# Performance work log

Hardware: AMD Instinct MI355X
Metric: run time of the kernel (lower is better)

The kernel has to match this reference:

```python
import jax, jax.numpy as jnp
import numpy as np

N_NODES = 50000
N_EDGES = 600000
N_GRAPHS = 64
IN_D, HID, EMB = 5, 128, 64
BN_EPS = 1e-5


def setup_inputs() -> dict:
    key = jax.random.key(0)
    ks = jax.random.split(key, 16)
    x = jax.random.normal(ks[0], (N_NODES, IN_D), dtype=jnp.float32)
    src = jax.random.randint(ks[1], (N_EDGES,), 0, N_NODES, dtype=jnp.int32)
    dst = jax.random.randint(ks[2], (N_EDGES,), 0, N_NODES, dtype=jnp.int32)
    batch = jnp.sort(jax.random.randint(ks[3], (N_NODES,), 0, N_GRAPHS, dtype=jnp.int32))
    def lin(k, fi, fo):
        s = 1.0 / np.sqrt(fi)
        kw, kb = jax.random.split(k)
        return (jax.random.uniform(kw, (fi, fo), jnp.float32, -s, s),
                jax.random.uniform(kb, (fo,), jnp.float32, -s, s))
    W1, b1 = lin(ks[4], IN_D, HID)
    W2, b2 = lin(ks[5], HID, HID)
    W3, b3 = lin(ks[6], HID, HID)
    Wp, bp = lin(ks[7], HID, EMB)
    g1 = 1.0 + 0.1 * jax.random.normal(ks[8], (HID,), jnp.float32)
    g2 = 1.0 + 0.1 * jax.random.normal(ks[9], (HID,), jnp.float32)
    g3 = 1.0 + 0.1 * jax.random.normal(ks[10], (HID,), jnp.float32)
    be1 = 0.1 * jax.random.normal(ks[11], (HID,), jnp.float32)
    be2 = 0.1 * jax.random.normal(ks[12], (HID,), jnp.float32)
    be3 = 0.1 * jax.random.normal(ks[13], (HID,), jnp.float32)
    return dict(x=x, src=src, dst=dst, batch=batch,
                W1=W1, b1=b1, W2=W2, b2=b2, W3=W3, b3=b3,
                g1=g1, be1=be1, g2=g2, be2=be2, g3=g3, be3=be3,
                Wp=Wp, bp=bp)


def reference(x, src, dst, batch, W1, b1, W2, b2, W3, b3,
              g1, be1, g2, be2, g3, be3, Wp, bp):
    n = x.shape[0]
    # GCNConv with self-loops and symmetric normalization (PyG default)
    loop = jnp.arange(n, dtype=src.dtype)
    s = jnp.concatenate([src, loop])
    d = jnp.concatenate([dst, loop])
    deg = jax.ops.segment_sum(jnp.ones_like(d, dtype=x.dtype), d, num_segments=n)
    dinv = jnp.where(deg > 0, jax.lax.rsqrt(deg), 0.0)
    norm = (dinv[s] * dinv[d])[:, None]  # (E+N, 1)

    def gcn(h, W, b):
        hw = h @ W                                   # (N, HID)
        msg = hw[s] * norm                           # gather + scale
        agg = jax.ops.segment_sum(msg, d, num_segments=n)
        return agg + b

    def bn_relu(h, g, be):
        # eval-mode BatchNorm1d with running_mean=0, running_var=1
        return jax.nn.relu(h * (g * jax.lax.rsqrt(jnp.asarray(1.0 + BN_EPS, h.dtype))) + be)

    h = bn_relu(gcn(x, W1, b1), g1, be1)
    h = bn_relu(gcn(h, W2, b2), g2, be2)
    h = bn_relu(gcn(h, W3, b3), g3, be3)

    # global mean pool over graphs
    sums = jax.ops.segment_sum(h, batch, num_segments=N_GRAPHS)
    cnt = jax.ops.segment_sum(jnp.ones((n,), h.dtype), batch, num_segments=N_GRAPHS)
    pooled = sums / jnp.maximum(cnt, 1.0)[:, None]
    return pooled @ Wp + bp
```

## Files before the change

kernel.cpp:

```cpp
#include <hip/hip_runtime.h>
#include <hip/hip_fp16.h>

#define N_NODES 50000
#define N_EDGES 600000
#define N_GRAPHS 64
#define IN_D 5
#define HID 128
#define EMB 64

#define CHUNK 512
#define NCHUNK ((N_NODES + CHUNK - 1) / CHUNK)
#define NREP 16
#define NLOC 4

typedef _Float16 half8 __attribute__((ext_vector_type(8)));
typedef float float4v __attribute__((ext_vector_type(4)));


__global__ __launch_bounds__(256) void k_init(
        int* __restrict__ cnt, int* __restrict__ fill, float* __restrict__ psum_rep,
        const float* __restrict__ W2, const float* __restrict__ W3,
        _Float16* __restrict__ Wt2, _Float16* __restrict__ Wt3) {
    int tid = blockIdx.x * blockDim.x + threadIdx.x;
    int nt = gridDim.x * blockDim.x;
    for (int i = tid; i < N_NODES; i += nt) { cnt[i] = 0; fill[i] = 0; }
    for (int i = tid; i < NREP * N_GRAPHS * HID; i += nt) psum_rep[i] = 0.f;
    for (int i = tid; i < 2 * HID * HID; i += nt) {
        int rem = i & (HID * HID - 1);
        int k = rem & 127, f = rem >> 7;
        if (i < HID * HID) Wt2[rem] = (_Float16)W2[k * HID + f];
        else               Wt3[rem] = (_Float16)W3[k * HID + f];
    }
}


__global__ __launch_bounds__(256) void k_count(
        const int* __restrict__ dst, int* __restrict__ cnt) {
    int e = blockIdx.x * blockDim.x + threadIdx.x;
    if (e < N_EDGES) atomicAdd(&cnt[dst[e]], 1);
}


__global__ void k_chunksum(const int* __restrict__ cnt, int* __restrict__ csum,
                           float* __restrict__ dinv) {
    __shared__ int sh[256];
    int b = blockIdx.x, t = threadIdx.x;
    int i0 = b * CHUNK + t, i1 = i0 + 256;
    int v = 0;
    if (i0 < N_NODES) { int c = cnt[i0]; v += c; dinv[i0] = rsqrtf((float)c + 1.0f); }
    if (i1 < N_NODES) { int c = cnt[i1]; v += c; dinv[i1] = rsqrtf((float)c + 1.0f); }
    sh[t] = v; __syncthreads();
    for (int off = 128; off > 0; off >>= 1) {
        if (t < off) sh[t] += sh[t + off];
        __syncthreads();
    }
    if (t == 0) csum[b] = sh[0];
}


__global__ void k_scan(const int* __restrict__ cnt, const int* __restrict__ csum,
                       int* __restrict__ row_start) {
    __shared__ int ws[4];
    int b = blockIdx.x, t = threadIdx.x;
    int lane = t & 63, w = t >> 6;

    int pre = 0;
    for (int j = lane; j < b; j += 64) pre += csum[j];
    #pragma unroll
    for (int off = 32; off > 0; off >>= 1) pre += __shfl_down(pre, off);
    pre = __shfl(pre, 0);

    int base = b * CHUNK;
    int i0 = base + 2 * t, i1 = i0 + 1;
    int c0 = (i0 < N_NODES) ? cnt[i0] : 0;
    int c1 = (i1 < N_NODES) ? cnt[i1] : 0;
    int v = c0 + c1;
    int s = v;
    #pragma unroll
    for (int off = 1; off < 64; off <<= 1) {
        int u = __shfl_up(s, off);
        if (lane >= off) s += u;
    }
    if (lane == 63) ws[w] = s;
    __syncthreads();
    if (t == 0) {
        int r = 0;
        #pragma unroll
        for (int j = 0; j < 4; ++j) { int xx = ws[j]; ws[j] = r; r += xx; }
    }
    __syncthreads();
    int excl = s - v + ws[w] + pre;
    if (i0 < N_NODES) row_start[i0] = excl;
    if (i1 < N_NODES) row_start[i1] = excl + c0;
    if (b == 0 && t == 0) row_start[N_NODES] = N_EDGES;
}


__global__ __launch_bounds__(256) void k_scatter(
        const int* __restrict__ src, const int* __restrict__ dst,
        const float* __restrict__ dinv, const int* __restrict__ row_start,
        int* __restrict__ fill, int2* __restrict__ e_pack) {
    int e = blockIdx.x * blockDim.x + threadIdx.x;
    if (e >= N_EDGES) return;
    int d = dst[e];
    int pos = row_start[d] + atomicAdd(&fill[d], 1);
    int s = src[e];
    e_pack[pos] = make_int2(s, __float_as_int(dinv[s]));
}


__global__ __launch_bounds__(256) void k_agg5g1(
        const float* __restrict__ x, const float* __restrict__ dinv,
        const int* __restrict__ row_start, const int2* __restrict__ e_pack,
        const float* __restrict__ W1, const float* __restrict__ b1,
        const float* __restrict__ g1, const float* __restrict__ be1,
        __half2* __restrict__ H16) {
    int gid = blockIdx.x * blockDim.x + threadIdx.x;
    int i = gid >> 3, k = gid & 7;
    if (i >= N_NODES) return;
    float acc = 0.f;
    if (k < IN_D) {
        int beg = row_start[i], end = row_start[i + 1];
        int e = beg;
        for (; e + 3 < end; e += 4) {
            int2 p0 = e_pack[e];
            int2 p1 = e_pack[e + 1];
            int2 p2 = e_pack[e + 2];
            int2 p3 = e_pack[e + 3];
            float x0 = x[p0.x * IN_D + k];
            float x1 = x[p1.x * IN_D + k];
            float x2 = x[p2.x * IN_D + k];
            float x3 = x[p3.x * IN_D + k];
            acc = fmaf(__int_as_float(p0.y), x0, acc);
            acc = fmaf(__int_as_float(p1.y), x1, acc);
            acc = fmaf(__int_as_float(p2.y), x2, acc);
            acc = fmaf(__int_as_float(p3.y), x3, acc);
        }
        for (; e < end; ++e) {
            int2 p = e_pack[e];
            acc = fmaf(__int_as_float(p.y), x[p.x * IN_D + k], acc);
        }
        float di = dinv[i];
        acc = di * (acc + di * x[i * IN_D + k]);
    }
    int lane = threadIdx.x & 63;
    int base = lane & ~7;
    float a0 = __shfl(acc, base + 0);
    float a1 = __shfl(acc, base + 1);
    float a2 = __shfl(acc, base + 2);
    float a3 = __shfl(acc, base + 3);
    float a4 = __shfl(acc, base + 4);
    const float rs = rsqrtf(1.0f + 1e-5f);
    int f0 = k * 16;
    #pragma unroll
    for (int u = 0; u < 8; ++u) {
        int fa = f0 + u * 2, fb = fa + 1;
        float va = b1[fa], vb = b1[fb];
        va = fmaf(a0, W1[0 * HID + fa], va); vb = fmaf(a0, W1[0 * HID + fb], vb);
        va = fmaf(a1, W1[1 * HID + fa], va); vb = fmaf(a1, W1[1 * HID + fb], vb);
        va = fmaf(a2, W1[2 * HID + fa], va); vb = fmaf(a2, W1[2 * HID + fb], vb);
        va = fmaf(a3, W1[3 * HID + fa], va); vb = fmaf(a3, W1[3 * HID + fb], vb);
        va = fmaf(a4, W1[4 * HID + fa], va); vb = fmaf(a4, W1[4 * HID + fb], vb);
        va = fmaf(va, g1[fa] * rs, be1[fa]);
        vb = fmaf(vb, g1[fb] * rs, be1[fb]);
        va = va > 0.f ? va : 0.f;
        vb = vb > 0.f ? vb : 0.f;
        H16[(size_t)i * 64 + k * 8 + u] = __floats2half2_rn(va, vb);
    }
}


__global__ __launch_bounds__(256) void k_agg128h(
        const __half2* __restrict__ H2, const float* __restrict__ dinv,
        const int* __restrict__ row_start, const int2* __restrict__ e_pack,
        __half2* __restrict__ A16) {
    int n = (blockIdx.x * blockDim.x + threadIdx.x) >> 6;
    int lane = threadIdx.x & 63;
    if (n >= N_NODES) return;
    float2 acc = make_float2(0.f, 0.f);
    int beg = row_start[n], end = row_start[n + 1];
    int e = beg;
    for (; e + 7 < end; e += 8) {
        int2 p[8];
        float2 h[8];
        #pragma unroll
        for (int u = 0; u < 8; ++u) p[u] = e_pack[e + u];
        #pragma unroll
        for (int u = 0; u < 8; ++u)
            h[u] = __half22float2(H2[(size_t)p[u].x * 64 + lane]);
        #pragma unroll
        for (int u = 0; u < 8; ++u) {
            float w = __int_as_float(p[u].y);
            acc.x = fmaf(w, h[u].x, acc.x);
            acc.y = fmaf(w, h[u].y, acc.y);
        }
    }
    for (; e + 3 < end; e += 4) {
        int2 p[4];
        float2 h[4];
        #pragma unroll
        for (int u = 0; u < 4; ++u) p[u] = e_pack[e + u];
        #pragma unroll
        for (int u = 0; u < 4; ++u)
            h[u] = __half22float2(H2[(size_t)p[u].x * 64 + lane]);
        #pragma unroll
        for (int u = 0; u < 4; ++u) {
            float w = __int_as_float(p[u].y);
            acc.x = fmaf(w, h[u].x, acc.x);
            acc.y = fmaf(w, h[u].y, acc.y);
        }
    }
    for (; e < end; ++e) {
        int2 pe = e_pack[e];
        float w = __int_as_float(pe.y);
        float2 f = __half22float2(H2[(size_t)pe.x * 64 + lane]);
        acc.x = fmaf(w, f.x, acc.x);
        acc.y = fmaf(w, f.y, acc.y);
    }
    float di = dinv[n];
    float2 hs = __half22float2(H2[(size_t)n * 64 + lane]);
    acc.x = fmaf(di, hs.x, acc.x);
    acc.y = fmaf(di, hs.y, acc.y);
    A16[(size_t)n * 64 + lane] = __floats2half2_rn(di * acc.x, di * acc.y);
}


__global__ __launch_bounds__(256) void k_gemm2(
        const _Float16* __restrict__ A16, const _Float16* __restrict__ Wt,
        const float* __restrict__ bb, const float* __restrict__ gg,
        const float* __restrict__ bee, _Float16* __restrict__ outH) {
    int t = threadIdx.x;
    int w = t >> 6, lane = t & 63;
    int quad = lane >> 4, r16 = lane & 15;
    int nb = blockIdx.x * 64 + w * 16;
    const float rs = rsqrtf(1.0f + 1e-5f);
    const half8* Arow = (const half8*)(A16 + (size_t)(nb + r16) * 128);
    half8 a[4];
    #pragma unroll
    for (int kb = 0; kb < 4; ++kb) a[kb] = Arow[kb * 4 + quad];
    #pragma unroll
    for (int ft = 0; ft < 8; ++ft) {
        int f = ft * 16 + r16;
        const half8* Brow = (const half8*)(Wt + (size_t)f * 128);
        float4v acc = {0.f, 0.f, 0.f, 0.f};
        #pragma unroll
        for (int kb = 0; kb < 4; ++kb)
            acc = __builtin_amdgcn_mfma_f32_16x16x32_f16(a[kb], Brow[kb * 4 + quad],
                                                         acc, 0, 0, 0);
        float b0 = bb[f], g0 = gg[f] * rs, e0 = bee[f];
        #pragma unroll
        for (int rr = 0; rr < 4; ++rr) {
            int n = nb + quad * 4 + rr;
            if (n < N_NODES) {
                float v = fmaf(acc[rr] + b0, g0, e0);
                v = v > 0.f ? v : 0.f;
                outH[(size_t)n * 128 + f] = (_Float16)v;
            }
        }
    }
}


__global__ __launch_bounds__(256) void k_gemm3pool(
        const _Float16* __restrict__ A16, const _Float16* __restrict__ Wt,
        const float* __restrict__ bb, const float* __restrict__ gg,
        const float* __restrict__ bee, const int* __restrict__ batch,
        float* __restrict__ psum_rep) {
    __shared__ float sh_pool[NLOC][HID];
    int t = threadIdx.x;
    int w = t >> 6, lane = t & 63;
    int quad = lane >> 4, r16 = lane & 15;
    int blk = (int)blockIdx.x;
    int nb = blk * 64 + w * 16;
    const float rs = rsqrtf(1.0f + 1e-5f);

    for (int i = t; i < NLOC * HID; i += 256) ((float*)sh_pool)[i] = 0.f;

    const half8* Arow = (const half8*)(A16 + (size_t)(nb + r16) * 128);
    half8 a[4];
    #pragma unroll
    for (int kb = 0; kb < 4; ++kb) a[kb] = Arow[kb * 4 + quad];

    int nb0 = blk * 64;
    if (nb0 > N_NODES - 1) nb0 = N_NODES - 1;
    int g0 = batch[nb0];
    int gi4[4];
    #pragma unroll
    for (int rr = 0; rr < 4; ++rr) {
        int n = nb + quad * 4 + rr;
        gi4[rr] = (n < N_NODES) ? batch[n] : -1;
    }
    __syncthreads();

    float* rep = psum_rep + (size_t)(blk & (NREP - 1)) * N_GRAPHS * HID;

    #pragma unroll
    for (int ft = 0; ft < 8; ++ft) {
        int f = ft * 16 + r16;
        const half8* Brow = (const half8*)(Wt + (size_t)f * 128);
        float4v acc = {0.f, 0.f, 0.f, 0.f};
        #pragma unroll
        for (int kb = 0; kb < 4; ++kb)
            acc = __builtin_amdgcn_mfma_f32_16x16x32_f16(a[kb], Brow[kb * 4 + quad],
                                                         acc, 0, 0, 0);
        float b0 = bb[f], g0f = gg[f] * rs, e0 = bee[f];
        float partial = 0.f;
        int cur = -1;
        #pragma unroll
        for (int rr = 0; rr < 4; ++rr) {
            int gi = gi4[rr];
            if (gi >= 0) {
                float v = fmaf(acc[rr] + b0, g0f, e0);
                v = v > 0.f ? v : 0.f;
                if (gi != cur) {
                    if (cur >= 0) {
                        int idx = cur - g0;
                        if (idx < NLOC) atomicAdd(&sh_pool[idx][f], partial);
                        else            atomicAdd(&rep[cur * HID + f], partial);
                    }
                    partial = 0.f; cur = gi;
                }
                partial += v;
            }
        }
        if (cur >= 0) {
            int idx = cur - g0;
            if (idx < NLOC) atomicAdd(&sh_pool[idx][f], partial);
            else            atomicAdd(&rep[cur * HID + f], partial);
        }
    }
    __syncthreads();
    for (int i = t; i < NLOC * HID; i += 256) {
        int idx = i >> 7, f = i & 127;
        float v = sh_pool[idx][f];
        int g = g0 + idx;
        if (v != 0.f && g < N_GRAPHS) atomicAdd(&rep[g * HID + f], v);
    }
}


__device__ __forceinline__ int lower_bound_batch(const int* __restrict__ batch, int val) {
    int lo = 0, hi = N_NODES;
    while (lo < hi) {
        int mid = (lo + hi) >> 1;
        if (batch[mid] < val) lo = mid + 1;
        else hi = mid;
    }
    return lo;
}

__global__ void k_final(const float* __restrict__ psum_rep, const int* __restrict__ batch,
                        const float* __restrict__ Wp, const float* __restrict__ bp,
                        float* __restrict__ out) {
    __shared__ float s_p[HID];
    int gi = blockIdx.x, e = threadIdx.x;
    for (int f = e; f < HID; f += EMB) {
        float v = 0.f;
        #pragma unroll
        for (int r = 0; r < NREP; ++r)
            v += psum_rep[(size_t)r * N_GRAPHS * HID + gi * HID + f];
        s_p[f] = v;
    }
    int lane = e & 63;
    int r = 0;
    if (lane < 2) r = lower_bound_batch(batch, gi + lane);
    int c0 = __shfl(r, 0), c1 = __shfl(r, 1);
    float inv = 1.0f / fmaxf((float)(c1 - c0), 1.0f);
    __syncthreads();
    float acc = bp[e];
    #pragma unroll 8
    for (int f = 0; f < HID; ++f)
        acc = fmaf(s_p[f] * inv, Wp[f * EMB + e], acc);
    out[gi * EMB + e] = acc;
}


extern "C" void kernel_launch(void* const* d_in, const int* in_sizes, int n_in,
                              void* d_out, int out_size, void* d_ws, size_t ws_size,
                              hipStream_t stream) {
    const float* x   = (const float*)d_in[0];
    const int*   src = (const int*)d_in[1];
    const int*   dst = (const int*)d_in[2];
    const int* batch = (const int*)d_in[3];
    const float* W1 = (const float*)d_in[4];
    const float* b1 = (const float*)d_in[5];
    const float* W2 = (const float*)d_in[6];
    const float* b2 = (const float*)d_in[7];
    const float* W3 = (const float*)d_in[8];
    const float* b3 = (const float*)d_in[9];
    const float* g1 = (const float*)d_in[10];
    const float* be1 = (const float*)d_in[11];
    const float* g2 = (const float*)d_in[12];
    const float* be2 = (const float*)d_in[13];
    const float* g3 = (const float*)d_in[14];
    const float* be3 = (const float*)d_in[15];
    const float* Wp = (const float*)d_in[16];
    const float* bp = (const float*)d_in[17];
    float* out = (float*)d_out;

    char* ws = (char*)d_ws;
    size_t o = 0;
    auto alloc = [&](size_t bytes) {
        void* pp = ws + o;
        o += bytes;
        o = (o + 255) & ~255ull;
        return pp;
    };
    int*      cnt       = (int*)alloc(N_NODES * 4);
    int*      fill      = (int*)alloc(N_NODES * 4);
    int*      row_start = (int*)alloc((N_NODES + 1) * 4);
    int*      csum      = (int*)alloc(NCHUNK * 4);
    float*    dinv      = (float*)alloc(N_NODES * 4);
    int2*     e_pack    = (int2*)alloc((size_t)N_EDGES * 8);
    _Float16* Wt2       = (_Float16*)alloc(HID * HID * 2);
    _Float16* Wt3       = (_Float16*)alloc(HID * HID * 2);
    __half2*  H16       = (__half2*)alloc((size_t)(N_NODES + 64) * HID * 2);
    __half2*  A16       = (__half2*)alloc((size_t)(N_NODES + 64) * HID * 2);
    float*    psum_rep  = (float*)alloc((size_t)NREP * N_GRAPHS * HID * 4);

    k_init<<<512, 256, 0, stream>>>(cnt, fill, psum_rep, W2, W3, Wt2, Wt3);
    k_count<<<(N_EDGES + 255) / 256, 256, 0, stream>>>(dst, cnt);
    k_chunksum<<<NCHUNK, 256, 0, stream>>>(cnt, csum, dinv);
    k_scan<<<NCHUNK, 256, 0, stream>>>(cnt, csum, row_start);
    k_scatter<<<(N_EDGES + 255) / 256, 256, 0, stream>>>(src, dst, dinv, row_start,
                                                         fill, e_pack);
    k_agg5g1<<<(N_NODES * 8 + 255) / 256, 256, 0, stream>>>(x, dinv, row_start, e_pack,
                                                            W1, b1, g1, be1, H16);
    k_agg128h<<<(N_NODES * 64 + 255) / 256, 256, 0, stream>>>(H16, dinv, row_start,
                                                              e_pack, A16);
    k_gemm2<<<(N_NODES + 63) / 64, 256, 0, stream>>>((const _Float16*)A16, Wt2,
                                                     b2, g2, be2, (_Float16*)H16);
    k_agg128h<<<(N_NODES * 64 + 255) / 256, 256, 0, stream>>>(H16, dinv, row_start,
                                                              e_pack, A16);
    k_gemm3pool<<<(N_NODES + 63) / 64, 256, 0, stream>>>((const _Float16*)A16, Wt3,
                                                         b3, g3, be3, batch, psum_rep);
    k_final<<<N_GRAPHS, EMB, 0, stream>>>(psum_rep, batch, Wp, bp, out);
}
```

Before: 293.9 us.

## Fuse 128-wide aggregation with MFMA GEMM through LDS and merge scan kernels

Each block now aggregates 64 nodes' neighbour features into padded shared memory and feeds them directly to the MFMA GEMM with BN/ReLU (and pooling in the last layer). This removes the A16 intermediate round-trip to global memory and two launches. The chunk-sum and scan kernels are merged into one kernel that recomputes prefixes directly, and init work is folded in alongside a memset. The cost is that each wave processes its 16 rows sequentially in the gather phase, which gives less memory parallelism per wave than the old one-node-per-wave layout, and the prefix loop is quadratic in the number of chunks.

```diff
diff --git a/kernel.cpp b/kernel.cpp
--- a/kernel.cpp
+++ b/kernel.cpp
@@ -12,26 +12,11 @@
 #define NCHUNK ((N_NODES + CHUNK - 1) / CHUNK)
 #define NREP 16
 #define NLOC 4
+#define RSTRIDE_H 136
 
 typedef _Float16 half8 __attribute__((ext_vector_type(8)));
+typedef _Float16 half2v __attribute__((ext_vector_type(2)));
 typedef float float4v __attribute__((ext_vector_type(4)));
-
-
-__global__ __launch_bounds__(256) void k_init(
-        int* __restrict__ cnt, int* __restrict__ fill, float* __restrict__ psum_rep,
-        const float* __restrict__ W2, const float* __restrict__ W3,
-        _Float16* __restrict__ Wt2, _Float16* __restrict__ Wt3) {
-    int tid = blockIdx.x * blockDim.x + threadIdx.x;
-    int nt = gridDim.x * blockDim.x;
-    for (int i = tid; i < N_NODES; i += nt) { cnt[i] = 0; fill[i] = 0; }
-    for (int i = tid; i < NREP * N_GRAPHS * HID; i += nt) psum_rep[i] = 0.f;
-    for (int i = tid; i < 2 * HID * HID; i += nt) {
-        int rem = i & (HID * HID - 1);
-        int k = rem & 127, f = rem >> 7;
-        if (i < HID * HID) Wt2[rem] = (_Float16)W2[k * HID + f];
-        else               Wt3[rem] = (_Float16)W3[k * HID + f];
-    }
-}
 
 
 __global__ __launch_bounds__(256) void k_count(
@@ -41,36 +26,27 @@
 }
 
 
-__global__ void k_chunksum(const int* __restrict__ cnt, int* __restrict__ csum,
-                           float* __restrict__ dinv) {
+__global__ __launch_bounds__(256) void k_scan2(
+        const int* __restrict__ cnt, int* __restrict__ row_start,
+        float* __restrict__ dinv, int* __restrict__ fill,
+        float* __restrict__ psum_rep,
+        const float* __restrict__ W2, const float* __restrict__ W3,
+        _Float16* __restrict__ Wt2, _Float16* __restrict__ Wt3) {
     __shared__ int sh[256];
+    __shared__ int ws[4];
     int b = blockIdx.x, t = threadIdx.x;
-    int i0 = b * CHUNK + t, i1 = i0 + 256;
-    int v = 0;
-    if (i0 < N_NODES) { int c = cnt[i0]; v += c; dinv[i0] = rsqrtf((float)c + 1.0f); }
-    if (i1 < N_NODES) { int c = cnt[i1]; v += c; dinv[i1] = rsqrtf((float)c + 1.0f); }
-    sh[t] = v; __syncthreads();
+    int lane = t & 63, w = t >> 6;
+    int base = b * CHUNK;
+
+    int part = 0;
+    for (int j = t; j < base; j += 256) part += cnt[j];
+    sh[t] = part; __syncthreads();
     for (int off = 128; off > 0; off >>= 1) {
         if (t < off) sh[t] += sh[t + off];
         __syncthreads();
     }
-    if (t == 0) csum[b] = sh[0];
-}
-
-
-__global__ void k_scan(const int* __restrict__ cnt, const int* __restrict__ csum,
-                       int* __restrict__ row_start) {
-    __shared__ int ws[4];
-    int b = blockIdx.x, t = threadIdx.x;
-    int lane = t & 63, w = t >> 6;
-
-    int pre = 0;
-    for (int j = lane; j < b; j += 64) pre += csum[j];
-    #pragma unroll
-    for (int off = 32; off > 0; off >>= 1) pre += __shfl_down(pre, off);
-    pre = __shfl(pre, 0);
-
-    int base = b * CHUNK;
+    int pre = sh[0];
+
     int i0 = base + 2 * t, i1 = i0 + 1;
     int c0 = (i0 < N_NODES) ? cnt[i0] : 0;
     int c1 = (i1 < N_NODES) ? cnt[i1] : 0;
@@ -90,9 +66,20 @@
     }
     __syncthreads();
     int excl = s - v + ws[w] + pre;
-    if (i0 < N_NODES) row_start[i0] = excl;
-    if (i1 < N_NODES) row_start[i1] = excl + c0;
+    if (i0 < N_NODES) { row_start[i0] = excl;      dinv[i0] = rsqrtf((float)c0 + 1.0f); }
+    if (i1 < N_NODES) { row_start[i1] = excl + c0; dinv[i1] = rsqrtf((float)c1 + 1.0f); }
     if (b == 0 && t == 0) row_start[N_NODES] = N_EDGES;
+
+    int gt = b * 256 + t;
+    const int NT = NCHUNK * 256;
+    for (int i = gt; i < N_NODES; i += NT) fill[i] = 0;
+    for (int i = gt; i < NREP * N_GRAPHS * HID; i += NT) psum_rep[i] = 0.f;
+    for (int i = gt; i < 2 * HID * HID; i += NT) {
+        int rem = i & (HID * HID - 1);
+        int k = rem & 127, f = rem >> 7;
+        if (i < HID * HID) Wt2[rem] = (_Float16)W2[k * HID + f];
+        else               Wt3[rem] = (_Float16)W3[k * HID + f];
+    }
 }
 
 
@@ -170,129 +157,100 @@
 }
 
 
-__global__ __launch_bounds__(256) void k_agg128h(
-        const __half2* __restrict__ H2, const float* __restrict__ dinv,
+template <bool POOL>
+__global__ __launch_bounds__(256) void k_fuse(
+        const __half2* __restrict__ Hsrc, const float* __restrict__ dinv,
         const int* __restrict__ row_start, const int2* __restrict__ e_pack,
-        __half2* __restrict__ A16) {
-    int n = (blockIdx.x * blockDim.x + threadIdx.x) >> 6;
-    int lane = threadIdx.x & 63;
-    if (n >= N_NODES) return;
-    float2 acc = make_float2(0.f, 0.f);
-    int beg = row_start[n], end = row_start[n + 1];
-    int e = beg;
-    for (; e + 7 < end; e += 8) {
-        int2 p[8];
-        float2 h[8];
-        #pragma unroll
-        for (int u = 0; u < 8; ++u) p[u] = e_pack[e + u];
-        #pragma unroll
-        for (int u = 0; u < 8; ++u)
-            h[u] = __half22float2(H2[(size_t)p[u].x * 64 + lane]);
-        #pragma unroll
-        for (int u = 0; u < 8; ++u) {
-            float w = __int_as_float(p[u].y);
-            acc.x = fmaf(w, h[u].x, acc.x);
-            acc.y = fmaf(w, h[u].y, acc.y);
-        }
-    }
-    for (; e + 3 < end; e += 4) {
-        int2 p[4];
-        float2 h[4];
-        #pragma unroll
-        for (int u = 0; u < 4; ++u) p[u] = e_pack[e + u];
-        #pragma unroll
-        for (int u = 0; u < 4; ++u)
-            h[u] = __half22float2(H2[(size_t)p[u].x * 64 + lane]);
-        #pragma unroll
-        for (int u = 0; u < 4; ++u) {
-            float w = __int_as_float(p[u].y);
-            acc.x = fmaf(w, h[u].x, acc.x);
-            acc.y = fmaf(w, h[u].y, acc.y);
-        }
-    }
-    for (; e < end; ++e) {
-        int2 pe = e_pack[e];
-        float w = __int_as_float(pe.y);
-        float2 f = __half22float2(H2[(size_t)pe.x * 64 + lane]);
-        acc.x = fmaf(w, f.x, acc.x);
-        acc.y = fmaf(w, f.y, acc.y);
-    }
-    float di = dinv[n];
-    float2 hs = __half22float2(H2[(size_t)n * 64 + lane]);
-    acc.x = fmaf(di, hs.x, acc.x);
-    acc.y = fmaf(di, hs.y, acc.y);
-    A16[(size_t)n * 64 + lane] = __floats2half2_rn(di * acc.x, di * acc.y);
-}
-
-
-__global__ __launch_bounds__(256) void k_gemm2(
-        const _Float16* __restrict__ A16, const _Float16* __restrict__ Wt,
-        const float* __restrict__ bb, const float* __restrict__ gg,
-        const float* __restrict__ bee, _Float16* __restrict__ outH) {
+        const _Float16* __restrict__ Wt, const float* __restrict__ bb,
+        const float* __restrict__ gg, const float* __restrict__ bee,
+        _Float16* __restrict__ Hdst,
+        const int* __restrict__ batch, float* __restrict__ psum_rep) {
+    __shared__ _Float16 shA[4 * 16 * RSTRIDE_H];
+    __shared__ float sh_pool[NLOC][HID];
     int t = threadIdx.x;
     int w = t >> 6, lane = t & 63;
+    int blk = (int)blockIdx.x;
+    const float rs = rsqrtf(1.0f + 1e-5f);
+
+    int g0 = 0;
+    if (POOL) {
+        for (int i = t; i < NLOC * HID; i += 256) ((float*)sh_pool)[i] = 0.f;
+        int nb0 = blk * 64;
+        if (nb0 > N_NODES - 1) nb0 = N_NODES - 1;
+        g0 = batch[nb0];
+        __syncthreads();
+    }
+
+    _Float16* myA = shA + w * 16 * RSTRIDE_H;
+    for (int r = 0; r < 16; ++r) {
+        int n = blk * 64 + w * 16 + r;
+        float2 acc = make_float2(0.f, 0.f);
+        if (n < N_NODES) {
+            int beg = row_start[n], end = row_start[n + 1];
+            int e = beg;
+            for (; e + 7 < end; e += 8) {
+                int2 p[8];
+                float2 h[8];
+                #pragma unroll
+                for (int u = 0; u < 8; ++u) p[u] = e_pack[e + u];
+                #pragma unroll
+                for (int u = 0; u < 8; ++u)
+                    h[u] = __half22float2(Hsrc[(size_t)p[u].x * 64 + lane]);
+                #pragma unroll
+                for (int u = 0; u < 8; ++u) {
+                    float wt = __int_as_float(p[u].y);
+                    acc.x = fmaf(wt, h[u].x, acc.x);
+                    acc.y = fmaf(wt, h[u].y, acc.y);
+                }
+            }
+            for (; e + 3 < end; e += 4) {
+                int2 p[4];
+                float2 h[4];
+                #pragma unroll
+                for (int u = 0; u < 4; ++u) p[u] = e_pack[e + u];
+                #pragma unroll
+                for (int u = 0; u < 4; ++u)
+                    h[u] = __half22float2(Hsrc[(size_t)p[u].x * 64 + lane]);
+                #pragma unroll
+                for (int u = 0; u < 4; ++u) {
+                    float wt = __int_as_float(p[u].y);
+                    acc.x = fmaf(wt, h[u].x, acc.x);
+                    acc.y = fmaf(wt, h[u].y, acc.y);
+                }
+            }
+            for (; e < end; ++e) {
+                int2 pe = e_pack[e];
+                float wt = __int_as_float(pe.y);
+                float2 f = __half22float2(Hsrc[(size_t)pe.x * 64 + lane]);
+                acc.x = fmaf(wt, f.x, acc.x);
+                acc.y = fmaf(wt, f.y, acc.y);
+            }
+            float di = dinv[n];
+            float2 hs = __half22float2(Hsrc[(size_t)n * 64 + lane]);
+            acc.x = di * fmaf(di, hs.x, acc.x);
+            acc.y = di * fmaf(di, hs.y, acc.y);
+        }
+        half2v hv = { (_Float16)acc.x, (_Float16)acc.y };
+        *(half2v*)(myA + r * RSTRIDE_H + lane * 2) = hv;
+    }
+
     int quad = lane >> 4, r16 = lane & 15;
-    int nb = blockIdx.x * 64 + w * 16;
-    const float rs = rsqrtf(1.0f + 1e-5f);
-    const half8* Arow = (const half8*)(A16 + (size_t)(nb + r16) * 128);
+    int nb = blk * 64 + w * 16;
+    const _Float16* rowp = myA + r16 * RSTRIDE_H;
     half8 a[4];
     #pragma unroll
-    for (int kb = 0; kb < 4; ++kb) a[kb] = Arow[kb * 4 + quad];
-    #pragma unroll
-    for (int ft = 0; ft < 8; ++ft) {
-        int f = ft * 16 + r16;
-        const half8* Brow = (const half8*)(Wt + (size_t)f * 128);
-        float4v acc = {0.f, 0.f, 0.f, 0.f};
-        #pragma unroll
-        for (int kb = 0; kb < 4; ++kb)
-            acc = __builtin_amdgcn_mfma_f32_16x16x32_f16(a[kb], Brow[kb * 4 + quad],
-                                                         acc, 0, 0, 0);
-        float b0 = bb[f], g0 = gg[f] * rs, e0 = bee[f];
+    for (int kb = 0; kb < 4; ++kb)
+        a[kb] = *(const half8*)(rowp + kb * 32 + quad * 8);
+
+    int gi4[4];
+    if (POOL) {
         #pragma unroll
         for (int rr = 0; rr < 4; ++rr) {
             int n = nb + quad * 4 + rr;
-            if (n < N_NODES) {
-                float v = fmaf(acc[rr] + b0, g0, e0);
-                v = v > 0.f ? v : 0.f;
-                outH[(size_t)n * 128 + f] = (_Float16)v;
-            }
-        }
-    }
-}
-
-
-__global__ __launch_bounds__(256) void k_gemm3pool(
-        const _Float16* __restrict__ A16, const _Float16* __restrict__ Wt,
-        const float* __restrict__ bb, const float* __restrict__ gg,
-        const float* __restrict__ bee, const int* __restrict__ batch,
-        float* __restrict__ psum_rep) {
-    __shared__ float sh_pool[NLOC][HID];
-    int t = threadIdx.x;
-    int w = t >> 6, lane = t & 63;
-    int quad = lane >> 4, r16 = lane & 15;
-    int blk = (int)blockIdx.x;
-    int nb = blk * 64 + w * 16;
-    const float rs = rsqrtf(1.0f + 1e-5f);
-
-    for (int i = t; i < NLOC * HID; i += 256) ((float*)sh_pool)[i] = 0.f;
-
-    const half8* Arow = (const half8*)(A16 + (size_t)(nb + r16) * 128);
-    half8 a[4];
-    #pragma unroll
-    for (int kb = 0; kb < 4; ++kb) a[kb] = Arow[kb * 4 + quad];
-
-    int nb0 = blk * 64;
-    if (nb0 > N_NODES - 1) nb0 = N_NODES - 1;
-    int g0 = batch[nb0];
-    int gi4[4];
-    #pragma unroll
-    for (int rr = 0; rr < 4; ++rr) {
-        int n = nb + quad * 4 + rr;
-        gi4[rr] = (n < N_NODES) ? batch[n] : -1;
-    }
-    __syncthreads();
-
-    float* rep = psum_rep + (size_t)(blk & (NREP - 1)) * N_GRAPHS * HID;
+            gi4[rr] = (n < N_NODES) ? batch[n] : -1;
+        }
+    }
+    float* rep = POOL ? (psum_rep + (size_t)(blk & (NREP - 1)) * N_GRAPHS * HID) : nullptr;
 
     #pragma unroll
     for (int ft = 0; ft < 8; ++ft) {
@@ -304,37 +262,52 @@
             acc = __builtin_amdgcn_mfma_f32_16x16x32_f16(a[kb], Brow[kb * 4 + quad],
                                                          acc, 0, 0, 0);
         float b0 = bb[f], g0f = gg[f] * rs, e0 = bee[f];
-        float partial = 0.f;
-        int cur = -1;
-        #pragma unroll
-        for (int rr = 0; rr < 4; ++rr) {
-            int gi = gi4[rr];
-            if (gi >= 0) {
-                float v = fmaf(acc[rr] + b0, g0f, e0);
-                v = v > 0.f ? v : 0.f;
-                if (gi != cur) {
-                    if (cur >= 0) {
-                        int idx = cur - g0;
-                        if (idx < NLOC) atomicAdd(&sh_pool[idx][f], partial);
-                        else            atomicAdd(&rep[cur * HID + f], partial);
+        if (POOL) {
+            float partial = 0.f;
+            int cur = -1;
+            #pragma unroll
+            for (int rr = 0; rr < 4; ++rr) {
+                int gi = gi4[rr];
+                if (gi >= 0) {
+                    float v = fmaf(acc[rr] + b0, g0f, e0);
+                    v = v > 0.f ? v : 0.f;
+                    if (gi != cur) {
+                        if (cur >= 0) {
+                            int idx = cur - g0;
+                            if (idx < NLOC) atomicAdd(&sh_pool[idx][f], partial);
+                            else            atomicAdd(&rep[cur * HID + f], partial);
+                        }
+                        partial = 0.f; cur = gi;
                     }
-                    partial = 0.f; cur = gi;
+                    partial += v;
                 }
-                partial += v;
-            }
-        }
-        if (cur >= 0) {
-            int idx = cur - g0;
-            if (idx < NLOC) atomicAdd(&sh_pool[idx][f], partial);
-            else            atomicAdd(&rep[cur * HID + f], partial);
-        }
-    }
-    __syncthreads();
-    for (int i = t; i < NLOC * HID; i += 256) {
-        int idx = i >> 7, f = i & 127;
-        float v = sh_pool[idx][f];
-        int g = g0 + idx;
-        if (v != 0.f && g < N_GRAPHS) atomicAdd(&rep[g * HID + f], v);
+            }
+            if (cur >= 0) {
+                int idx = cur - g0;
+                if (idx < NLOC) atomicAdd(&sh_pool[idx][f], partial);
+                else            atomicAdd(&rep[cur * HID + f], partial);
+            }
+        } else {
+            #pragma unroll
+            for (int rr = 0; rr < 4; ++rr) {
+                int n = nb + quad * 4 + rr;
+                if (n < N_NODES) {
+                    float v = fmaf(acc[rr] + b0, g0f, e0);
+                    v = v > 0.f ? v : 0.f;
+                    Hdst[(size_t)n * 128 + f] = (_Float16)v;
+                }
+            }
+        }
+    }
+
+    if (POOL) {
+        __syncthreads();
+        for (int i = t; i < NLOC * HID; i += 256) {
+            int idx = i >> 7, f = i & 127;
+            float v = sh_pool[idx][f];
+            int g = g0 + idx;
+            if (v != 0.f && g < N_GRAPHS) atomicAdd(&rep[g * HID + f], v);
+        }
     }
 }
 
@@ -409,30 +382,27 @@
     int*      cnt       = (int*)alloc(N_NODES * 4);
     int*      fill      = (int*)alloc(N_NODES * 4);
     int*      row_start = (int*)alloc((N_NODES + 1) * 4);
-    int*      csum      = (int*)alloc(NCHUNK * 4);
     float*    dinv      = (float*)alloc(N_NODES * 4);
     int2*     e_pack    = (int2*)alloc((size_t)N_EDGES * 8);
     _Float16* Wt2       = (_Float16*)alloc(HID * HID * 2);
     _Float16* Wt3       = (_Float16*)alloc(HID * HID * 2);
     __half2*  H16       = (__half2*)alloc((size_t)(N_NODES + 64) * HID * 2);
-    __half2*  A16       = (__half2*)alloc((size_t)(N_NODES + 64) * HID * 2);
+    __half2*  H16b      = (__half2*)alloc((size_t)(N_NODES + 64) * HID * 2);
     float*    psum_rep  = (float*)alloc((size_t)NREP * N_GRAPHS * HID * 4);
 
-    k_init<<<512, 256, 0, stream>>>(cnt, fill, psum_rep, W2, W3, Wt2, Wt3);
+    hipMemsetAsync(cnt, 0, N_NODES * 4, stream);
     k_count<<<(N_EDGES + 255) / 256, 256, 0, stream>>>(dst, cnt);
-    k_chunksum<<<NCHUNK, 256, 0, stream>>>(cnt, csum, dinv);
-    k_scan<<<NCHUNK, 256, 0, stream>>>(cnt, csum, row_start);
+    k_scan2<<<NCHUNK, 256, 0, stream>>>(cnt, row_start, dinv, fill, psum_rep,
+                                        W2, W3, Wt2, Wt3);
     k_scatter<<<(N_EDGES + 255) / 256, 256, 0, stream>>>(src, dst, dinv, row_start,
                                                          fill, e_pack);
     k_agg5g1<<<(N_NODES * 8 + 255) / 256, 256, 0, stream>>>(x, dinv, row_start, e_pack,
                                                             W1, b1, g1, be1, H16);
-    k_agg128h<<<(N_NODES * 64 + 255) / 256, 256, 0, stream>>>(H16, dinv, row_start,
-                                                              e_pack, A16);
-    k_gemm2<<<(N_NODES + 63) / 64, 256, 0, stream>>>((const _Float16*)A16, Wt2,
-                                                     b2, g2, be2, (_Float16*)H16);
-    k_agg128h<<<(N_NODES * 64 + 255) / 256, 256, 0, stream>>>(H16, dinv, row_start,
-                                                              e_pack, A16);
-    k_gemm3pool<<<(N_NODES + 63) / 64, 256, 0, stream>>>((const _Float16*)A16, Wt3,
-                                                         b3, g3, be3, batch, psum_rep);
+    k_fuse<false><<<(N_NODES + 63) / 64, 256, 0, stream>>>(
+        H16, dinv, row_start, e_pack, Wt2, b2, g2, be2,
+        (_Float16*)H16b, nullptr, nullptr);
+    k_fuse<true><<<(N_NODES + 63) / 64, 256, 0, stream>>>(
+        H16b, dinv, row_start, e_pack, Wt3, b3, g3, be3,
+        nullptr, batch, psum_rep);
     k_final<<<N_GRAPHS, EMB, 0, stream>>>(psum_rep, batch, Wp, bp, out);
 }
```

New measurement: 333.7 us. 1.14x slower.

## Merge chunk-sum and scan kernels, fold init work into scan kernel

Applied to the files above, without the earlier changes.

Replaces the separate chunk-sum and scan kernels with one kernel in which each block sums every count before its chunk, so no second pass over per-chunk sums is needed. The init of fill, psum_rep and the fp16 weight transposes moves into that scan kernel, and the count buffer is zeroed with a memset. The goal is fewer kernel launches and less launch overhead in the preprocessing phase. In exchange, every block now reads the whole prefix of the count array, which is quadratic total reads (about 98 blocks times up to 50K ints), and the init work is spread over fewer threads.

```diff
diff --git a/kernel.cpp b/kernel.cpp
--- a/kernel.cpp
+++ b/kernel.cpp
@@ -17,23 +17,6 @@
 typedef float float4v __attribute__((ext_vector_type(4)));
 
 
-__global__ __launch_bounds__(256) void k_init(
-        int* __restrict__ cnt, int* __restrict__ fill, float* __restrict__ psum_rep,
-        const float* __restrict__ W2, const float* __restrict__ W3,
-        _Float16* __restrict__ Wt2, _Float16* __restrict__ Wt3) {
-    int tid = blockIdx.x * blockDim.x + threadIdx.x;
-    int nt = gridDim.x * blockDim.x;
-    for (int i = tid; i < N_NODES; i += nt) { cnt[i] = 0; fill[i] = 0; }
-    for (int i = tid; i < NREP * N_GRAPHS * HID; i += nt) psum_rep[i] = 0.f;
-    for (int i = tid; i < 2 * HID * HID; i += nt) {
-        int rem = i & (HID * HID - 1);
-        int k = rem & 127, f = rem >> 7;
-        if (i < HID * HID) Wt2[rem] = (_Float16)W2[k * HID + f];
-        else               Wt3[rem] = (_Float16)W3[k * HID + f];
-    }
-}
-
-
 __global__ __launch_bounds__(256) void k_count(
         const int* __restrict__ dst, int* __restrict__ cnt) {
     int e = blockIdx.x * blockDim.x + threadIdx.x;
@@ -41,36 +24,27 @@
 }
 
 
-__global__ void k_chunksum(const int* __restrict__ cnt, int* __restrict__ csum,
-                           float* __restrict__ dinv) {
+__global__ __launch_bounds__(256) void k_scan2(
+        const int* __restrict__ cnt, int* __restrict__ row_start,
+        float* __restrict__ dinv, int* __restrict__ fill,
+        float* __restrict__ psum_rep,
+        const float* __restrict__ W2, const float* __restrict__ W3,
+        _Float16* __restrict__ Wt2, _Float16* __restrict__ Wt3) {
     __shared__ int sh[256];
+    __shared__ int ws[4];
     int b = blockIdx.x, t = threadIdx.x;
-    int i0 = b * CHUNK + t, i1 = i0 + 256;
-    int v = 0;
-    if (i0 < N_NODES) { int c = cnt[i0]; v += c; dinv[i0] = rsqrtf((float)c + 1.0f); }
-    if (i1 < N_NODES) { int c = cnt[i1]; v += c; dinv[i1] = rsqrtf((float)c + 1.0f); }
-    sh[t] = v; __syncthreads();
+    int lane = t & 63, w = t >> 6;
+    int base = b * CHUNK;
+
+    int part = 0;
+    for (int j = t; j < base; j += 256) part += cnt[j];
+    sh[t] = part; __syncthreads();
     for (int off = 128; off > 0; off >>= 1) {
         if (t < off) sh[t] += sh[t + off];
         __syncthreads();
     }
-    if (t == 0) csum[b] = sh[0];
-}
-
-
-__global__ void k_scan(const int* __restrict__ cnt, const int* __restrict__ csum,
-                       int* __restrict__ row_start) {
-    __shared__ int ws[4];
-    int b = blockIdx.x, t = threadIdx.x;
-    int lane = t & 63, w = t >> 6;
-
-    int pre = 0;
-    for (int j = lane; j < b; j += 64) pre += csum[j];
-    #pragma unroll
-    for (int off = 32; off > 0; off >>= 1) pre += __shfl_down(pre, off);
-    pre = __shfl(pre, 0);
-
-    int base = b * CHUNK;
+    int pre = sh[0];
+
     int i0 = base + 2 * t, i1 = i0 + 1;
     int c0 = (i0 < N_NODES) ? cnt[i0] : 0;
     int c1 = (i1 < N_NODES) ? cnt[i1] : 0;
@@ -90,9 +64,20 @@
     }
     __syncthreads();
     int excl = s - v + ws[w] + pre;
-    if (i0 < N_NODES) row_start[i0] = excl;
-    if (i1 < N_NODES) row_start[i1] = excl + c0;
+    if (i0 < N_NODES) { row_start[i0] = excl;      dinv[i0] = rsqrtf((float)c0 + 1.0f); }
+    if (i1 < N_NODES) { row_start[i1] = excl + c0; dinv[i1] = rsqrtf((float)c1 + 1.0f); }
     if (b == 0 && t == 0) row_start[N_NODES] = N_EDGES;
+
+    int gt = b * 256 + t;
+    const int NT = NCHUNK * 256;
+    for (int i = gt; i < N_NODES; i += NT) fill[i] = 0;
+    for (int i = gt; i < NREP * N_GRAPHS * HID; i += NT) psum_rep[i] = 0.f;
+    for (int i = gt; i < 2 * HID * HID; i += NT) {
+        int rem = i & (HID * HID - 1);
+        int k = rem & 127, f = rem >> 7;
+        if (i < HID * HID) Wt2[rem] = (_Float16)W2[k * HID + f];
+        else               Wt3[rem] = (_Float16)W3[k * HID + f];
+    }
 }
 
 
@@ -409,7 +394,6 @@
     int*      cnt       = (int*)alloc(N_NODES * 4);
     int*      fill      = (int*)alloc(N_NODES * 4);
     int*      row_start = (int*)alloc((N_NODES + 1) * 4);
-    int*      csum      = (int*)alloc(NCHUNK * 4);
     float*    dinv      = (float*)alloc(N_NODES * 4);
     int2*     e_pack    = (int2*)alloc((size_t)N_EDGES * 8);
     _Float16* Wt2       = (_Float16*)alloc(HID * HID * 2);
@@ -418,10 +402,10 @@
     __half2*  A16       = (__half2*)alloc((size_t)(N_NODES + 64) * HID * 2);
     float*    psum_rep  = (float*)alloc((size_t)NREP * N_GRAPHS * HID * 4);
 
-    k_init<<<512, 256, 0, stream>>>(cnt, fill, psum_rep, W2, W3, Wt2, Wt3);
+    hipMemsetAsync(cnt, 0, N_NODES * 4, stream);
     k_count<<<(N_EDGES + 255) / 256, 256, 0, stream>>>(dst, cnt);
-    k_chunksum<<<NCHUNK, 256, 0, stream>>>(cnt, csum, dinv);
-    k_scan<<<NCHUNK, 256, 0, stream>>>(cnt, csum, row_start);
+    k_scan2<<<NCHUNK, 256, 0, stream>>>(cnt, row_start, dinv, fill, psum_rep,
+                                        W2, W3, Wt2, Wt3);
     k_scatter<<<(N_EDGES + 255) / 256, 256, 0, stream>>>(src, dst, dinv, row_start,
                                                          fill, e_pack);
     k_agg5g1<<<(N_NODES * 8 + 255) / 256, 256, 0, stream>>>(x, dinv, row_start, e_pack,
```

Result: slower. 315.1 us, median of 2 (+7.2%).
